# Optimization experiments

Measured on AMD Instinct MI355X. Metric: run time of the kernel, lower is better.

Reference implementation:

```python
import jax, jax.numpy as jnp
import numpy as np

N_NODES = 50000
N_EDGES = 800000
D = 128          # input_node_dim == output_node_dim (residual)
T = 3            # number of node types == number of edge types
NODE_IN = D + T * D  # node updater input dim = 512


def setup_inputs() -> dict:
    key = jax.random.key(0)
    ks = jax.random.split(key, 8)
    scale = 0.05
    return {
        "node_feature": jax.random.normal(ks[0], (N_NODES, D), jnp.float32),
        "W_e": jax.random.normal(ks[1], (T, D, D), jnp.float32) * scale,
        "b_e": jnp.zeros((T, D), jnp.float32),
        "W_n": jax.random.normal(ks[2], (T, D, NODE_IN), jnp.float32) * scale,
        "b_n": jnp.zeros((T, D), jnp.float32),
        "edge_src": jax.random.randint(ks[3], (N_EDGES,), 0, N_NODES, jnp.int32),
        "edge_dst": jax.random.randint(ks[4], (N_EDGES,), 0, N_NODES, jnp.int32),
        "edge_type": jax.random.randint(ks[5], (N_EDGES,), 0, T, jnp.int32),
        "node_type": jax.random.randint(ks[6], (N_NODES,), 0, T, jnp.int32),
    }


def reference(node_feature, W_e, b_e, W_n, b_n, edge_src, edge_dst, edge_type, node_type):
    N, Din = node_feature.shape
    n_types = W_e.shape[0]
    out_dim = W_e.shape[1]

    # message_function: per-edge-type MLP on source features, relu, zero elsewhere
    src = node_feature[edge_src]                      # [E, D] gather
    parts = [jax.nn.relu(node_feature)]               # reduce_function relu's node_feature
    for t in range(n_types):
        msg = jax.nn.relu(src @ W_e[t].T + b_e[t])    # [E, out]
        msg = jnp.where((edge_type == t)[:, None], msg, jnp.zeros((), msg.dtype))
        # mailbox sum over incoming edges per destination node
        parts.append(jax.ops.segment_sum(msg, edge_dst, num_segments=N))
    agg = jnp.concatenate(parts, axis=1)              # [N, D + T*out]

    # per-node-type updater MLP, dispatched by node_type
    updated = jnp.zeros((N, out_dim), node_feature.dtype)
    for t in range(n_types):
        o = agg @ W_n[t].T + b_n[t]                   # [N, out]
        updated = jnp.where((node_type == t)[:, None], o, updated)

    # use_residual = True
    return updated + node_feature
```

## Files before the change

### kernel.cpp

```cpp
#include <hip/hip_runtime.h>
#include <hip/hip_bf16.h>

#define NN 50000
#define NE 800000
#define DD 128
#define NT 3
#define AGGW 384
#define EM 64
#define EM2 128
#define LDK 136
#define CB 32
#define LDK2 520
#define NBITS 7
#define NBINS ((NN + 127) / 128)
#define EPB 2048
#define BINCAP 2560
#define NTILES_MAX (((NN + EM - 1) / EM) + NT)
#define NTILE_PAD (((NTILES_MAX + 7) / 8) * 8)

typedef __bf16 bf16x8 __attribute__((ext_vector_type(8)));
typedef float f32x4 __attribute__((ext_vector_type(4)));
typedef unsigned short u16x8 __attribute__((ext_vector_type(8)));

__device__ __forceinline__ unsigned short f2b(float f) {
    __hip_bfloat16 h = __float2bfloat16(f);
    return __builtin_bit_cast(unsigned short, h);
}
__device__ __forceinline__ float b2f(unsigned int u16bits) {
    unsigned int x = u16bits << 16;
    return __builtin_bit_cast(float, x);
}

__global__ void k_zero(int* __restrict__ bhist, int* __restrict__ cnts) {
    int i = blockIdx.x * blockDim.x + threadIdx.x;
    if (i < NBINS) bhist[i] = 0;
    if (i >= NBINS && i < NBINS + 16) cnts[i - NBINS] = 0;
}

__global__ void k_prep(const float* __restrict__ nf, const float* __restrict__ We,
                       const float* __restrict__ Wn, unsigned short* __restrict__ nfb,
                       unsigned short* __restrict__ Web, unsigned short* __restrict__ Wnb) {
    const size_t n0 = (size_t)NN * DD / 8;
    const size_t n1 = (size_t)NT * DD * DD / 8;
    const size_t n2 = (size_t)NT * DD * 512 / 8;
    size_t i = (size_t)blockIdx.x * blockDim.x + threadIdx.x;
    size_t total = n0 + n1 + n2;
    for (size_t p = i; p < total; p += (size_t)gridDim.x * blockDim.x) {
        const float* s; unsigned short* d; size_t off;
        if (p < n0)            { s = nf; d = nfb; off = p; }
        else if (p < n0 + n1)  { s = We; d = Web; off = p - n0; }
        else                   { s = Wn; d = Wnb; off = p - n0 - n1; }
        const float4* f4 = (const float4*)(s + off * 8);
        float4 x = f4[0], y = f4[1];
        u16x8 u = { f2b(x.x), f2b(x.y), f2b(x.z), f2b(x.w),
                    f2b(y.x), f2b(y.y), f2b(y.z), f2b(y.w) };
        *(u16x8*)(d + off * 8) = u;
    }
}

__global__ __launch_bounds__(256) void k_binhist(const int* __restrict__ edst,
        const int* __restrict__ ntp, int* __restrict__ bhist, int* __restrict__ cnts) {
    __shared__ int lh[NBINS];
    __shared__ int ln[3];
    int tid = threadIdx.x;
    for (int i = tid; i < NBINS; i += 256) lh[i] = 0;
    if (tid < 3) ln[tid] = 0;
    __syncthreads();
    int i0 = blockIdx.x * blockDim.x + tid;
    int stride = gridDim.x * blockDim.x;
    for (int p = i0; p < NE; p += stride) atomicAdd(&lh[edst[p] >> NBITS], 1);
    for (int p = i0; p < NN; p += stride) atomicAdd(&ln[ntp[p]], 1);
    __syncthreads();
    for (int i = tid; i < NBINS; i += 256) if (lh[i]) atomicAdd(&bhist[i], lh[i]);
    if (tid < 3) atomicAdd(&cnts[6 + tid], ln[tid]);
}

__global__ __launch_bounds__(512) void k_binscan(const int* __restrict__ bhist,
        int* __restrict__ binptr, int* __restrict__ bincur, int* __restrict__ rowptr) {
    __shared__ int sa[NBINS], sb[NBINS];
    int tid = threadIdx.x;
    if (tid < NBINS) sa[tid] = bhist[tid];
    __syncthreads();
    int flip = 0;
    for (int off = 1; off < NBINS; off <<= 1) {
        int* src = flip ? sb : sa;
        int* dst = flip ? sa : sb;
        if (tid < NBINS) dst[tid] = src[tid] + ((tid >= off) ? src[tid - off] : 0);
        __syncthreads();
        flip ^= 1;
    }
    int* inc = flip ? sb : sa;
    if (tid < NBINS) {
        int excl = (tid == 0) ? 0 : inc[tid - 1];
        binptr[tid] = excl;
        bincur[tid] = excl;
    }
    if (tid == 0) { binptr[NBINS] = NE; rowptr[NN] = NE; }
}

__global__ __launch_bounds__(256) void k_binscatter(const int* __restrict__ esrc,
        const int* __restrict__ edst, const int* __restrict__ et,
        const int* __restrict__ ntp, int* __restrict__ bincur, int* __restrict__ cnts,
        int* __restrict__ pe, int* __restrict__ sn) {
    const int NEB = (NE + EPB - 1) / EPB;
    __shared__ int lh[NBINS], gb[NBINS], lr[NBINS];
    __shared__ int lcnt[3], lbase[3];
    int tid = threadIdx.x, b = blockIdx.x;
    if (b < NEB) {
        for (int i = tid; i < NBINS; i += 256) { lh[i] = 0; lr[i] = 0; }
        __syncthreads();
        int e0 = b * EPB;
        for (int i = 0; i < EPB; i += 256) {
            int e = e0 + i + tid;
            if (e < NE) atomicAdd(&lh[edst[e] >> NBITS], 1);
        }
        __syncthreads();
        for (int i = tid; i < NBINS; i += 256)
            if (lh[i]) gb[i] = atomicAdd(&bincur[i], lh[i]);
        __syncthreads();
        for (int i = 0; i < EPB; i += 256) {
            int e = e0 + i + tid;
            if (e < NE) {
                int d = edst[e];
                int bin = d >> NBITS;
                int rank = atomicAdd(&lr[bin], 1);
                pe[gb[bin] + rank] = esrc[e] | (et[e] << 16) | ((d & 127) << 18);
            }
        }
    } else {
        if (tid < 3) lcnt[tid] = 0;
        __syncthreads();
        int p = (b - NEB) * 256 + tid;
        int t = -1, rank = 0;
        if (p < NN) { t = ntp[p]; rank = atomicAdd(&lcnt[t], 1); }
        __syncthreads();
        if (tid < 3) lbase[tid] = atomicAdd(&cnts[9 + tid], lcnt[tid]);
        __syncthreads();
        if (p < NN) {
            int c0 = cnts[6], c1 = cnts[7];
            int off = (t == 0) ? 0 : (t == 1) ? c0 : c0 + c1;
            sn[off + lbase[t] + rank] = p;
        }
    }
}

__global__ __launch_bounds__(256) void k_binsort(const int* __restrict__ binptr,
        int* __restrict__ pe, int* __restrict__ rowptr) {
    __shared__ int lcnt[128], lrk[128], lrp[128];
    __shared__ unsigned int sorted[BINCAP];
    int b = blockIdx.x, tid = threadIdx.x;
    int beg = binptr[b], end = binptr[b + 1];
    int cnt = min(end - beg, BINCAP);
    if (tid < 128) { lcnt[tid] = 0; lrk[tid] = 0; }
    __syncthreads();
    for (int e = tid; e < cnt; e += 256)
        atomicAdd(&lcnt[(pe[beg + e] >> 18) & 127], 1);
    __syncthreads();
    if (tid < 64) {
        int v = lcnt[2 * tid] + lcnt[2 * tid + 1];
        int s = v;
        for (int d = 1; d < 64; d <<= 1) {
            int u = __shfl_up(s, d);
            if (tid >= d) s += u;
        }
        int excl = s - v;
        lrp[2 * tid] = excl;
        lrp[2 * tid + 1] = excl + lcnt[2 * tid];
    }
    __syncthreads();
    if (tid < 128) {
        int node = b * 128 + tid;
        if (node < NN) rowptr[node] = beg + lrp[tid];
    }
    for (int e = tid; e < cnt; e += 256) {
        unsigned int p = pe[beg + e];
        int d = (p >> 18) & 127;
        int pos = lrp[d] + atomicAdd(&lrk[d], 1);
        sorted[pos] = p;
    }
    __syncthreads();
    for (int e = tid; e < cnt; e += 256) pe[beg + e] = sorted[e];
}

__global__ __launch_bounds__(512, 4) void k_msg(const unsigned short* __restrict__ nfb,
        const unsigned short* __restrict__ Web, const float* __restrict__ be,
        unsigned short* __restrict__ M) {
    __shared__ unsigned short Wsm[DD][LDK];
    const int TILES = (NN + EM2 - 1) / EM2;
    int b = blockIdx.x;
    int t = b / TILES, tile = b % TILES;
    int base = tile * EM2;
    int m = min(EM2, NN - base);
    int tid = threadIdx.x;
    {
        int row = tid >> 2, c0 = (tid & 3) * 32;
        const u16x8* src = (const u16x8*)(Web + ((size_t)t * DD + row) * DD + c0);
#pragma unroll
        for (int v = 0; v < 4; ++v) *(u16x8*)&Wsm[row][c0 + v * 8] = src[v];
    }
    __syncthreads();

    int wave = tid >> 6, l = tid & 63, lr = l & 15, kg = l >> 4;
    int arow = min(base + wave * 16 + lr, NN - 1);
    const u16x8* Arow = (const u16x8*)(nfb + (size_t)arow * DD);
    f32x4 acc[8];
#pragma unroll
    for (int n = 0; n < 8; n++) acc[n] = (f32x4){0.f, 0.f, 0.f, 0.f};
#pragma unroll
    for (int k0 = 0; k0 < DD; k0 += 32) {
        bf16x8 a = __builtin_bit_cast(bf16x8, Arow[(k0 >> 3) + kg]);
#pragma unroll
        for (int n = 0; n < 8; n++) {
            bf16x8 bb = *(const bf16x8*)&Wsm[n * 16 + lr][k0 + kg * 8];
            acc[n] = __builtin_amdgcn_mfma_f32_16x16x32_bf16(a, bb, acc[n], 0, 0, 0);
        }
    }
    unsigned short* Mt = M + (size_t)t * NN * DD;
#pragma unroll
    for (int n = 0; n < 8; n++) {
        int col = n * 16 + lr;
        float bias = be[t * DD + col];
#pragma unroll
        for (int r = 0; r < 4; r++) {
            int row = wave * 16 + kg * 4 + r;
            if (row < m) {
                float v = acc[n][r] + bias;
                Mt[(size_t)(base + row) * DD + col] = f2b(fmaxf(v, 0.f));
            }
        }
    }
}

__global__ __launch_bounds__(256) void k_agg(const unsigned short* __restrict__ M,
        const int* __restrict__ rowptr, const int* __restrict__ pe,
        unsigned short* __restrict__ aggb) {
    int wid = blockIdx.x * 4 + (threadIdx.x >> 6);
    int l = threadIdx.x & 63;
    if (wid >= NN) return;
    int beg = rowptr[wid], end = rowptr[wid + 1];
    const unsigned int* Mu = (const unsigned int*)M;
    float a0x = 0.f, a0y = 0.f, a1x = 0.f, a1y = 0.f, a2x = 0.f, a2y = 0.f;
    int e = beg;
    for (; e + 7 < end; e += 8) {
        unsigned int p[8], v[8];
#pragma unroll
        for (int j = 0; j < 8; ++j) p[j] = pe[e + j];
#pragma unroll
        for (int j = 0; j < 8; ++j)
            v[j] = Mu[(((size_t)((p[j] >> 16) & 3) * NN + (p[j] & 0xFFFF)) << 6) + l];
#pragma unroll
        for (int j = 0; j < 8; ++j) {
            int t = (p[j] >> 16) & 3;
            float lo = b2f(v[j] & 0xFFFF), hi = b2f(v[j] >> 16);
            if (t == 0) { a0x += lo; a0y += hi; }
            else if (t == 1) { a1x += lo; a1y += hi; }
            else { a2x += lo; a2y += hi; }
        }
    }
    for (; e < end; ++e) {
        unsigned int p0 = pe[e];
        int t0 = (p0 >> 16) & 3;
        unsigned int v0 = Mu[(((size_t)t0 * NN + (p0 & 0xFFFF)) << 6) + l];
        float lo0 = b2f(v0 & 0xFFFF), hi0 = b2f(v0 >> 16);
        if (t0 == 0) { a0x += lo0; a0y += hi0; } else if (t0 == 1) { a1x += lo0; a1y += hi0; } else { a2x += lo0; a2y += hi0; }
    }
    unsigned int* dst = (unsigned int*)(aggb + (size_t)wid * AGGW);
    dst[l]       = (unsigned int)f2b(a0x) | ((unsigned int)f2b(a0y) << 16);
    dst[64 + l]  = (unsigned int)f2b(a1x) | ((unsigned int)f2b(a1y) << 16);
    dst[128 + l] = (unsigned int)f2b(a2x) | ((unsigned int)f2b(a2y) << 16);
}

__global__ __launch_bounds__(256, 3) void k_node(const float* __restrict__ nf,
        const unsigned short* __restrict__ nfb, const unsigned short* __restrict__ Wnb,
        const float* __restrict__ bn, const int* __restrict__ sn,
        const int* __restrict__ cnts, const unsigned short* __restrict__ aggb,
        float* __restrict__ out) {
    __shared__ unsigned short Wsm[CB][LDK2];
    int c0 = cnts[6], c1 = cnts[7], c2 = cnts[8];
    int n0 = (c0 + EM - 1) / EM, n1 = (c1 + EM - 1) / EM, n2 = (c2 + EM - 1) / EM;
    int ntile = n0 + n1 + n2;
    int b = blockIdx.x;
    int rt = (b & 7) * (NTILE_PAD / 8) + (b >> 3);
    if (rt >= ntile) return;
    int tid = threadIdx.x;
    int wave = tid >> 6, l = tid & 63, lr = l & 15, kg = l >> 4;
    int t, tile;
    if (rt < n0) { t = 0; tile = rt; }
    else if (rt < n0 + n1) { t = 1; tile = rt - n0; }
    else { t = 2; tile = rt - n0 - n1; }
    int off = (t == 0) ? 0 : (t == 1) ? c0 : c0 + c1;
    int cntt = (t == 0) ? c0 : (t == 1) ? c1 : c2;
    int base = off + tile * EM;
    int m = min(EM, cntt - tile * EM);

    int myrow = sn[base + min(wave * 16 + lr, m - 1)];
    const u16x8* An = (const u16x8*)(nfb + (size_t)myrow * DD);
    const u16x8* Ag = (const u16x8*)(aggb + (size_t)myrow * AGGW);
    u16x8 afr[16];
#pragma unroll
    for (int kc = 0; kc < 4; ++kc) {
#pragma unroll
        for (int k0 = 0; k0 < DD; k0 += 32) {
            u16x8 araw;
            if (kc == 0) {
                araw = An[(k0 >> 3) + kg];
#pragma unroll
                for (int j = 0; j < 8; ++j)
                    araw[j] = (araw[j] & 0x8000) ? (unsigned short)0 : araw[j];
            } else {
                araw = Ag[((kc - 1) * DD + k0) / 8 + kg];
            }
            afr[kc * 4 + (k0 >> 5)] = araw;
        }
    }

    int nd[4];
#pragma unroll
    for (int r = 0; r < 4; ++r) nd[r] = sn[base + min(wave * 16 + kg * 4 + r, m - 1)];

    int srow = tid & 31, scc = (tid >> 5) * 64;
#pragma unroll 1
    for (int cbk = 0; cbk < 4; ++cbk) {
        if (cbk) __syncthreads();
        const u16x8* src = (const u16x8*)(Wnb + ((size_t)t * DD + cbk * CB + srow) * 512 + scc);
#pragma unroll
        for (int v = 0; v < 8; ++v) *(u16x8*)&Wsm[srow][scc + v * 8] = src[v];
        __syncthreads();

        f32x4 acc0 = {0.f, 0.f, 0.f, 0.f}, acc1 = {0.f, 0.f, 0.f, 0.f};
#pragma unroll
        for (int kc = 0; kc < 4; ++kc) {
#pragma unroll
            for (int k0 = 0; k0 < DD; k0 += 32) {
                bf16x8 a = __builtin_bit_cast(bf16x8, afr[kc * 4 + (k0 >> 5)]);
                int kw = kc * DD + k0 + kg * 8;
                bf16x8 b0 = *(const bf16x8*)&Wsm[lr][kw];
                bf16x8 b1 = *(const bf16x8*)&Wsm[16 + lr][kw];
                acc0 = __builtin_amdgcn_mfma_f32_16x16x32_bf16(a, b0, acc0, 0, 0, 0);
                acc1 = __builtin_amdgcn_mfma_f32_16x16x32_bf16(a, b1, acc1, 0, 0, 0);
            }
        }
#pragma unroll
        for (int n = 0; n < 2; n++) {
            int col = cbk * CB + n * 16 + lr;
            float bias = bn[t * DD + col];
            const f32x4& av = n ? acc1 : acc0;
#pragma unroll
            for (int r = 0; r < 4; r++) {
                int row = wave * 16 + kg * 4 + r;
                if (row < m) {
                    int node = nd[r];
                    out[(size_t)node * DD + col] = av[r] + bias + nf[(size_t)node * DD + col];
                }
            }
        }
    }
}

extern "C" void kernel_launch(void* const* d_in, const int* in_sizes, int n_in,
                              void* d_out, int out_size, void* d_ws, size_t ws_size,
                              hipStream_t stream) {
    const float* nf   = (const float*)d_in[0];
    const float* We   = (const float*)d_in[1];
    const float* be   = (const float*)d_in[2];
    const float* Wn   = (const float*)d_in[3];
    const float* bn   = (const float*)d_in[4];
    const int*   esrc = (const int*)d_in[5];
    const int*   edst = (const int*)d_in[6];
    const int*   et   = (const int*)d_in[7];
    const int*   ntp  = (const int*)d_in[8];
    float* out = (float*)d_out;

    char* w = (char*)d_ws;
    unsigned short* M    = (unsigned short*)w;  w += (size_t)NT * NN * DD * 2;
    unsigned short* aggb = (unsigned short*)w;  w += (size_t)NN * AGGW * 2;
    unsigned short* nfb  = (unsigned short*)w;  w += (size_t)NN * DD * 2;
    unsigned short* Web  = (unsigned short*)w;  w += (size_t)NT * DD * DD * 2;
    unsigned short* Wnb  = (unsigned short*)w;  w += (size_t)NT * DD * 512 * 2;
    int* pe     = (int*)w;  w += (size_t)NE * 4;
    int* bhist  = (int*)w;  w += (NBINS + 1) * 4;
    int* binptr = (int*)w;  w += (NBINS + 1) * 4;
    int* bincur = (int*)w;  w += (NBINS + 1) * 4;
    int* rowptr = (int*)w;  w += (size_t)(NN + 1) * 4;
    int* sn     = (int*)w;  w += (size_t)NN * 4;
    int* cnts   = (int*)w;  w += 16 * 4;

    const int NEB = (NE + EPB - 1) / EPB;
    const int NCH = (NN + 255) / 256;
    const int TILES2 = (NN + EM2 - 1) / EM2;

    k_zero<<<2, 256, 0, stream>>>(bhist, cnts);
    k_prep<<<1024, 256, 0, stream>>>(nf, We, Wn, nfb, Web, Wnb);
    k_binhist<<<256, 256, 0, stream>>>(edst, ntp, bhist, cnts);
    k_binscan<<<1, 512, 0, stream>>>(bhist, binptr, bincur, rowptr);
    k_binscatter<<<NEB + NCH, 256, 0, stream>>>(esrc, edst, et, ntp, bincur, cnts, pe, sn);
    k_binsort<<<NBINS, 256, 0, stream>>>(binptr, pe, rowptr);
    k_msg<<<NT * TILES2, 512, 0, stream>>>(nfb, Web, be, M);
    k_agg<<<(NN + 3) / 4, 256, 0, stream>>>(M, rowptr, pe, aggb);
    k_node<<<NTILE_PAD, 256, 0, stream>>>(nf, nfb, Wnb, bn, sn, cnts, aggb, out);
}
```

Baseline: 157.9 us.

## Bucket edges by (type, destination) so aggregation runs per type without branches

The edge sort now keys on (edge type, destination bin), producing a per-type CSR (rowptr2 with NT*NN rows). The aggregation kernel launches one wave per (type, node) pair and accumulates into a single pair of registers, with no per-edge type branching. The tail loop is replaced by two masked 4-wide passes. This triples the number of aggregation waves, each with shorter rows, which may hurt latency hiding. BINCAP is lowered to 1024, which could truncate unusually large bins, though per-type bins average about 680 edges.

```diff
diff --git a/kernel.cpp b/kernel.cpp
--- a/kernel.cpp
+++ b/kernel.cpp
@@ -13,8 +13,9 @@
 #define LDK2 520
 #define NBITS 7
 #define NBINS ((NN + 127) / 128)
+#define NBT (NT * NBINS)
 #define EPB 2048
-#define BINCAP 2560
+#define BINCAP 1024
 #define NTILES_MAX (((NN + EM - 1) / EM) + NT)
 #define NTILE_PAD (((NTILES_MAX + 7) / 8) * 8)
 
@@ -33,8 +34,8 @@
 
 __global__ void k_zero(int* __restrict__ bhist, int* __restrict__ cnts) {
     int i = blockIdx.x * blockDim.x + threadIdx.x;
-    if (i < NBINS) bhist[i] = 0;
-    if (i >= NBINS && i < NBINS + 16) cnts[i - NBINS] = 0;
+    if (i < NBT) bhist[i] = 0;
+    if (i >= NBT && i < NBT + 16) cnts[i - NBT] = 0;
 }
 
 __global__ void k_prep(const float* __restrict__ nf, const float* __restrict__ We,
@@ -59,43 +60,48 @@
 }
 
 __global__ __launch_bounds__(256) void k_binhist(const int* __restrict__ edst,
-        const int* __restrict__ ntp, int* __restrict__ bhist, int* __restrict__ cnts) {
-    __shared__ int lh[NBINS];
+        const int* __restrict__ et, const int* __restrict__ ntp,
+        int* __restrict__ bhist, int* __restrict__ cnts) {
+    __shared__ int lh[NBT];
     __shared__ int ln[3];
     int tid = threadIdx.x;
-    for (int i = tid; i < NBINS; i += 256) lh[i] = 0;
+    for (int i = tid; i < NBT; i += 256) lh[i] = 0;
     if (tid < 3) ln[tid] = 0;
     __syncthreads();
     int i0 = blockIdx.x * blockDim.x + tid;
     int stride = gridDim.x * blockDim.x;
-    for (int p = i0; p < NE; p += stride) atomicAdd(&lh[edst[p] >> NBITS], 1);
+    for (int p = i0; p < NE; p += stride)
+        atomicAdd(&lh[et[p] * NBINS + (edst[p] >> NBITS)], 1);
     for (int p = i0; p < NN; p += stride) atomicAdd(&ln[ntp[p]], 1);
     __syncthreads();
-    for (int i = tid; i < NBINS; i += 256) if (lh[i]) atomicAdd(&bhist[i], lh[i]);
+    for (int i = tid; i < NBT; i += 256) if (lh[i]) atomicAdd(&bhist[i], lh[i]);
     if (tid < 3) atomicAdd(&cnts[6 + tid], ln[tid]);
 }
 
 __global__ __launch_bounds__(512) void k_binscan(const int* __restrict__ bhist,
-        int* __restrict__ binptr, int* __restrict__ bincur, int* __restrict__ rowptr) {
-    __shared__ int sa[NBINS], sb[NBINS];
+        int* __restrict__ binptr, int* __restrict__ bincur, int* __restrict__ rowptr2) {
+    __shared__ int sa[512], sb[512];
     int tid = threadIdx.x;
-    if (tid < NBINS) sa[tid] = bhist[tid];
+    int b0 = tid * 3;
+    int x0 = (b0     < NBT) ? bhist[b0]     : 0;
+    int x1 = (b0 + 1 < NBT) ? bhist[b0 + 1] : 0;
+    int x2 = (b0 + 2 < NBT) ? bhist[b0 + 2] : 0;
+    sa[tid] = x0 + x1 + x2;
     __syncthreads();
     int flip = 0;
-    for (int off = 1; off < NBINS; off <<= 1) {
+    for (int off = 1; off < 512; off <<= 1) {
         int* src = flip ? sb : sa;
         int* dst = flip ? sa : sb;
-        if (tid < NBINS) dst[tid] = src[tid] + ((tid >= off) ? src[tid - off] : 0);
+        dst[tid] = src[tid] + ((tid >= off) ? src[tid - off] : 0);
         __syncthreads();
         flip ^= 1;
     }
     int* inc = flip ? sb : sa;
-    if (tid < NBINS) {
-        int excl = (tid == 0) ? 0 : inc[tid - 1];
-        binptr[tid] = excl;
-        bincur[tid] = excl;
-    }
-    if (tid == 0) { binptr[NBINS] = NE; rowptr[NN] = NE; }
+    int excl = (tid == 0) ? 0 : inc[tid - 1];
+    if (b0     < NBT) { binptr[b0]     = excl;           bincur[b0]     = excl; }
+    if (b0 + 1 < NBT) { binptr[b0 + 1] = excl + x0;      bincur[b0 + 1] = excl + x0; }
+    if (b0 + 2 < NBT) { binptr[b0 + 2] = excl + x0 + x1; bincur[b0 + 2] = excl + x0 + x1; }
+    if (tid == 0) { binptr[NBT] = NE; rowptr2[NT * NN] = NE; }
 }
 
 __global__ __launch_bounds__(256) void k_binscatter(const int* __restrict__ esrc,
@@ -103,28 +109,29 @@
         const int* __restrict__ ntp, int* __restrict__ bincur, int* __restrict__ cnts,
         int* __restrict__ pe, int* __restrict__ sn) {
     const int NEB = (NE + EPB - 1) / EPB;
-    __shared__ int lh[NBINS], gb[NBINS], lr[NBINS];
+    __shared__ int lh[NBT], gb[NBT], lr[NBT];
     __shared__ int lcnt[3], lbase[3];
     int tid = threadIdx.x, b = blockIdx.x;
     if (b < NEB) {
-        for (int i = tid; i < NBINS; i += 256) { lh[i] = 0; lr[i] = 0; }
+        for (int i = tid; i < NBT; i += 256) { lh[i] = 0; lr[i] = 0; }
         __syncthreads();
         int e0 = b * EPB;
         for (int i = 0; i < EPB; i += 256) {
             int e = e0 + i + tid;
-            if (e < NE) atomicAdd(&lh[edst[e] >> NBITS], 1);
-        }
-        __syncthreads();
-        for (int i = tid; i < NBINS; i += 256)
+            if (e < NE) atomicAdd(&lh[et[e] * NBINS + (edst[e] >> NBITS)], 1);
+        }
+        __syncthreads();
+        for (int i = tid; i < NBT; i += 256)
             if (lh[i]) gb[i] = atomicAdd(&bincur[i], lh[i]);
         __syncthreads();
         for (int i = 0; i < EPB; i += 256) {
             int e = e0 + i + tid;
             if (e < NE) {
                 int d = edst[e];
-                int bin = d >> NBITS;
+                int t = et[e];
+                int bin = t * NBINS + (d >> NBITS);
                 int rank = atomicAdd(&lr[bin], 1);
-                pe[gb[bin] + rank] = esrc[e] | (et[e] << 16) | ((d & 127) << 18);
+                pe[gb[bin] + rank] = (t * NN + esrc[e]) | ((d & 127) << 18);
             }
         }
     } else {
@@ -145,10 +152,11 @@
 }
 
 __global__ __launch_bounds__(256) void k_binsort(const int* __restrict__ binptr,
-        int* __restrict__ pe, int* __restrict__ rowptr) {
+        int* __restrict__ pe, int* __restrict__ rowptr2) {
     __shared__ int lcnt[128], lrk[128], lrp[128];
     __shared__ unsigned int sorted[BINCAP];
     int b = blockIdx.x, tid = threadIdx.x;
+    int t = b / NBINS, bin = b % NBINS;
     int beg = binptr[b], end = binptr[b + 1];
     int cnt = min(end - beg, BINCAP);
     if (tid < 128) { lcnt[tid] = 0; lrk[tid] = 0; }
@@ -169,8 +177,8 @@
     }
     __syncthreads();
     if (tid < 128) {
-        int node = b * 128 + tid;
-        if (node < NN) rowptr[node] = beg + lrp[tid];
+        int node = bin * 128 + tid;
+        if (node < NN) rowptr2[t * NN + node] = beg + lrp[tid];
     }
     for (int e = tid; e < cnt; e += 256) {
         unsigned int p = pe[beg + e];
@@ -232,42 +240,50 @@
 }
 
 __global__ __launch_bounds__(256) void k_agg(const unsigned short* __restrict__ M,
-        const int* __restrict__ rowptr, const int* __restrict__ pe,
+        const int* __restrict__ rowptr2, const int* __restrict__ pe,
         unsigned short* __restrict__ aggb) {
-    int wid = blockIdx.x * 4 + (threadIdx.x >> 6);
+    const int BPT = NN / 4;
+    int b = blockIdx.x;
+    int t = b / BPT;
+    int node = (b - t * BPT) * 4 + (threadIdx.x >> 6);
     int l = threadIdx.x & 63;
-    if (wid >= NN) return;
-    int beg = rowptr[wid], end = rowptr[wid + 1];
+    int rix = t * NN + node;
+    int beg = rowptr2[rix], end = rowptr2[rix + 1];
     const unsigned int* Mu = (const unsigned int*)M;
-    float a0x = 0.f, a0y = 0.f, a1x = 0.f, a1y = 0.f, a2x = 0.f, a2y = 0.f;
+    float ax = 0.f, ay = 0.f;
     int e = beg;
-    for (; e + 7 < end; e += 8) {
+    for (; e + 8 <= end; e += 8) {
         unsigned int p[8], v[8];
 #pragma unroll
         for (int j = 0; j < 8; ++j) p[j] = pe[e + j];
 #pragma unroll
-        for (int j = 0; j < 8; ++j)
-            v[j] = Mu[(((size_t)((p[j] >> 16) & 3) * NN + (p[j] & 0xFFFF)) << 6) + l];
+        for (int j = 0; j < 8; ++j) v[j] = Mu[((p[j] & 0x3FFFFu) << 6) | l];
 #pragma unroll
         for (int j = 0; j < 8; ++j) {
-            int t = (p[j] >> 16) & 3;
-            float lo = b2f(v[j] & 0xFFFF), hi = b2f(v[j] >> 16);
-            if (t == 0) { a0x += lo; a0y += hi; }
-            else if (t == 1) { a1x += lo; a1y += hi; }
-            else { a2x += lo; a2y += hi; }
-        }
-    }
-    for (; e < end; ++e) {
-        unsigned int p0 = pe[e];
-        int t0 = (p0 >> 16) & 3;
-        unsigned int v0 = Mu[(((size_t)t0 * NN + (p0 & 0xFFFF)) << 6) + l];
-        float lo0 = b2f(v0 & 0xFFFF), hi0 = b2f(v0 >> 16);
-        if (t0 == 0) { a0x += lo0; a0y += hi0; } else if (t0 == 1) { a1x += lo0; a1y += hi0; } else { a2x += lo0; a2y += hi0; }
-    }
-    unsigned int* dst = (unsigned int*)(aggb + (size_t)wid * AGGW);
-    dst[l]       = (unsigned int)f2b(a0x) | ((unsigned int)f2b(a0y) << 16);
-    dst[64 + l]  = (unsigned int)f2b(a1x) | ((unsigned int)f2b(a1y) << 16);
-    dst[128 + l] = (unsigned int)f2b(a2x) | ((unsigned int)f2b(a2y) << 16);
+            ax += __builtin_bit_cast(float, v[j] << 16);
+            ay += __builtin_bit_cast(float, v[j] & 0xFFFF0000u);
+        }
+    }
+#pragma unroll 1
+    for (int pass = 0; pass < 2; ++pass) {
+        if (e < end) {
+            unsigned int p[4], v[4];
+#pragma unroll
+            for (int j = 0; j < 4; ++j) p[j] = pe[min(e + j, end - 1)];
+#pragma unroll
+            for (int j = 0; j < 4; ++j) v[j] = Mu[((p[j] & 0x3FFFFu) << 6) | l];
+#pragma unroll
+            for (int j = 0; j < 4; ++j) {
+                if (e + j < end) {
+                    ax += __builtin_bit_cast(float, v[j] << 16);
+                    ay += __builtin_bit_cast(float, v[j] & 0xFFFF0000u);
+                }
+            }
+            e += 4;
+        }
+    }
+    unsigned int* dst = (unsigned int*)aggb + (size_t)node * 192 + t * 64 + l;
+    *dst = (unsigned int)f2b(ax) | ((unsigned int)f2b(ay) << 16);
 }
 
 __global__ __launch_bounds__(256, 3) void k_node(const float* __restrict__ nf,
@@ -378,10 +394,10 @@
     unsigned short* Web  = (unsigned short*)w;  w += (size_t)NT * DD * DD * 2;
     unsigned short* Wnb  = (unsigned short*)w;  w += (size_t)NT * DD * 512 * 2;
     int* pe     = (int*)w;  w += (size_t)NE * 4;
-    int* bhist  = (int*)w;  w += (NBINS + 1) * 4;
-    int* binptr = (int*)w;  w += (NBINS + 1) * 4;
-    int* bincur = (int*)w;  w += (NBINS + 1) * 4;
-    int* rowptr = (int*)w;  w += (size_t)(NN + 1) * 4;
+    int* bhist  = (int*)w;  w += (NBT + 1) * 4;
+    int* binptr = (int*)w;  w += (NBT + 1) * 4;
+    int* bincur = (int*)w;  w += (NBT + 1) * 4;
+    int* rowptr2= (int*)w;  w += (size_t)(NT * NN + 1) * 4;
     int* sn     = (int*)w;  w += (size_t)NN * 4;
     int* cnts   = (int*)w;  w += 16 * 4;
 
@@ -389,13 +405,13 @@
     const int NCH = (NN + 255) / 256;
     const int TILES2 = (NN + EM2 - 1) / EM2;
 
-    k_zero<<<2, 256, 0, stream>>>(bhist, cnts);
+    k_zero<<<5, 256, 0, stream>>>(bhist, cnts);
     k_prep<<<1024, 256, 0, stream>>>(nf, We, Wn, nfb, Web, Wnb);
-    k_binhist<<<256, 256, 0, stream>>>(edst, ntp, bhist, cnts);
-    k_binscan<<<1, 512, 0, stream>>>(bhist, binptr, bincur, rowptr);
+    k_binhist<<<256, 256, 0, stream>>>(edst, et, ntp, bhist, cnts);
+    k_binscan<<<1, 512, 0, stream>>>(bhist, binptr, bincur, rowptr2);
     k_binscatter<<<NEB + NCH, 256, 0, stream>>>(esrc, edst, et, ntp, bincur, cnts, pe, sn);
-    k_binsort<<<NBINS, 256, 0, stream>>>(binptr, pe, rowptr);
+    k_binsort<<<NBT, 256, 0, stream>>>(binptr, pe, rowptr2);
     k_msg<<<NT * TILES2, 512, 0, stream>>>(nfb, Web, be, M);
-    k_agg<<<(NN + 3) / 4, 256, 0, stream>>>(M, rowptr, pe, aggb);
+    k_agg<<<NT * (NN / 4), 256, 0, stream>>>(M, rowptr2, pe, aggb);
     k_node<<<NTILE_PAD, 256, 0, stream>>>(nf, nfb, Wnb, bn, sn, cnts, aggb, out);
 }
```

New measurement: 178.5 us. 1.13x slower.
